# Optimization experiments

Measured on AMD Instinct MI355X. Metric: run time of the kernel, lower is better.

## Reference

```python
import jax, jax.numpy as jnp
import numpy as np

N = 50000      # nodes
E = 800000     # edges (avg degree 16)
C = 5000       # clusters (Kongming compression)
D = 128        # in_features
OUT = 40       # out_features (classes)
K = 2          # propagation hops


def setup_inputs() -> dict:
    key = jax.random.key(0)
    k1, k2, k3, k4, k5, k6 = jax.random.split(key, 6)
    x = jax.random.normal(k1, (N, D), dtype=jnp.float32)
    edge_index = jax.random.randint(k2, (2, E), 0, N, dtype=jnp.int32)
    cluster_index = jax.random.randint(k3, (N,), 0, C, dtype=jnp.int32)
    rep_idx = jax.random.randint(k4, (C,), 0, N, dtype=jnp.int32)
    W = jax.random.normal(k5, (OUT, D), dtype=jnp.float32) / np.sqrt(D)
    b = jax.random.normal(k6, (OUT,), dtype=jnp.float32) * 0.01
    return {"x": x, "edge_index": edge_index, "cluster_index": cluster_index,
            "rep_idx": rep_idx, "W": W, "b": b}


def _gcn_propagate(x, edge_index, k_hops):
    # PUPropagate: K hops of D^{-1/2}(A+I)D^{-1/2} x (gcn_norm with self-loops)
    n = x.shape[0]
    loops = jnp.arange(n, dtype=edge_index.dtype)
    src = jnp.concatenate([edge_index[0], loops])
    dst = jnp.concatenate([edge_index[1], loops])
    deg = jax.ops.segment_sum(jnp.ones_like(src, dtype=x.dtype), dst, num_segments=n)
    dinv = jnp.where(deg > 0, jax.lax.rsqrt(deg), 0.0)
    norm = (dinv[src] * dinv[dst])[:, None]            # [E+N, 1]
    h = x
    for _ in range(k_hops):                            # small fixed hop count
        h = jax.ops.segment_sum(h[src] * norm, dst, num_segments=n)
    return h


def reference(x, edge_index, cluster_index, rep_idx, W, b):
    h = _gcn_propagate(x, edge_index, K)               # [N, D]
    # Kongming_Cluster: gather one representative row per cluster
    hc = h[rep_idx]                                    # [C, D]
    yc = hc @ W.T + b                                  # [C, OUT] dense linear on compressed rows
    # Kongming_Reconstruct: scatter back to all nodes by cluster index
    y = yc[cluster_index]                              # [N, OUT]
    return jax.nn.log_softmax(y, axis=1)
```

## Files before the change

### kernel.cpp

```cpp
#include <hip/hip_runtime.h>
#include <math.h>

#define N_NODES 50000
#define N_EDGES 800000
#define N_CLUST 5000
#define DIM     128
#define NOUT    40
#define SLOTS   64
#define CSLOT   64

#define NBKT    391
#define BCAP    2560
#define GB_STR  16
#define BUCKB   250
#define EPB4    800

#define ZB     782
#define INVB   50
#define GRID_A (ZB + INVB + BUCKB)

typedef __attribute__((ext_vector_type(8))) short short8;
typedef __attribute__((ext_vector_type(4))) float fvec4;
typedef __attribute__((ext_vector_type(4))) int ivec4;

__device__ __forceinline__ short bf16r(float v) {
    unsigned u = __float_as_uint(v);
    u = (u + 0x7FFFu + ((u >> 16) & 1u)) >> 16;
    return (short)u;
}
__device__ __forceinline__ unsigned pack_bf16x2(float a, float b) {
    unsigned ua = __float_as_uint(a);
    unsigned ub = __float_as_uint(b);
    ua = (ua + 0x7FFFu + ((ua >> 16) & 1u)) >> 16;
    ub = (ub + 0x7FFFu + ((ub >> 16) & 1u)) >> 16;
    return ua | (ub << 16);
}
__device__ __forceinline__ float2 unpack_bf16x2(unsigned v) {
    float2 r;
    r.x = __uint_as_float(v << 16);
    r.y = __uint_as_float(v & 0xFFFF0000u);
    return r;
}
__device__ __forceinline__ float4 unpack_bf16x4(uint2 v) {
    float4 r;
    r.x = __uint_as_float(v.x << 16);
    r.y = __uint_as_float(v.x & 0xFFFF0000u);
    r.z = __uint_as_float(v.y << 16);
    r.w = __uint_as_float(v.y & 0xFFFF0000u);
    return r;
}
struct f8 { float4 a, b; };
__device__ __forceinline__ f8 unpack_bf16x8(uint4 q) {
    f8 r;
    r.a.x = __uint_as_float(q.x << 16);
    r.a.y = __uint_as_float(q.x & 0xFFFF0000u);
    r.a.z = __uint_as_float(q.y << 16);
    r.a.w = __uint_as_float(q.y & 0xFFFF0000u);
    r.b.x = __uint_as_float(q.z << 16);
    r.b.y = __uint_as_float(q.z & 0xFFFF0000u);
    r.b.z = __uint_as_float(q.w << 16);
    r.b.w = __uint_as_float(q.w & 0xFFFF0000u);
    return r;
}
__device__ __forceinline__ float4 sel4(bool c, float4 v) {
    float4 r;
    r.x = c ? v.x : 0.0f; r.y = c ? v.y : 0.0f;
    r.z = c ? v.z : 0.0f; r.w = c ? v.w : 0.0f;
    return r;
}

__global__ __launch_bounds__(256) void fused_A(const float* __restrict__ x,
                                               const int* __restrict__ esrc,
                                               const int* __restrict__ edst,
                                               const int* __restrict__ cidx,
                                               const float* __restrict__ W,
                                               int* __restrict__ ccnt,
                                               unsigned short* __restrict__ zs,
                                               unsigned short* __restrict__ cinv,
                                               int* __restrict__ gbcnt,
                                               unsigned* __restrict__ gbuck) {
    __shared__ int bcnt[NBKT];
    __shared__ int bbase[NBKT];
    int lane = threadIdx.x & 63;
    int wv = threadIdx.x >> 6;

    if (blockIdx.x < ZB) {
        int gw = blockIdx.x * 4 + wv;
        if (gw >= N_NODES / 16) return;
        int q = lane >> 4, r16 = lane & 15;

        short8 bfr[3][4];
        #pragma unroll
        for (int t = 0; t < 3; t++) {
            int o = t * 16 + r16;
            #pragma unroll
            for (int s = 0; s < 4; s++) {
                short8 f = {0, 0, 0, 0, 0, 0, 0, 0};
                if (o < NOUT) {
                    const float* wp = W + o * DIM + s * 32 + q * 8;
                    float4 w0 = *(const float4*)wp;
                    float4 w1 = *(const float4*)(wp + 4);
                    f[0] = bf16r(w0.x); f[1] = bf16r(w0.y);
                    f[2] = bf16r(w0.z); f[3] = bf16r(w0.w);
                    f[4] = bf16r(w1.x); f[5] = bf16r(w1.y);
                    f[6] = bf16r(w1.z); f[7] = bf16r(w1.w);
                }
                bfr[t][s] = f;
            }
        }

        int tile = gw;
        int node = tile * 16 + r16;
        short8 af[4];
        #pragma unroll
        for (int s = 0; s < 4; s++) {
            const fvec4* xp = (const fvec4*)(x + (size_t)node * DIM + s * 32 + q * 8);
            fvec4 a0 = *xp;
            fvec4 a1 = *(xp + 1);
            short8 f;
            f[0] = bf16r(a0.x); f[1] = bf16r(a0.y);
            f[2] = bf16r(a0.z); f[3] = bf16r(a0.w);
            f[4] = bf16r(a1.x); f[5] = bf16r(a1.y);
            f[6] = bf16r(a1.z); f[7] = bf16r(a1.w);
            af[s] = f;
        }

        fvec4 acc0 = {0, 0, 0, 0}, acc1 = {0, 0, 0, 0}, acc2 = {0, 0, 0, 0};
        #pragma unroll
        for (int s = 0; s < 4; s++) {
            acc0 = __builtin_amdgcn_mfma_f32_16x16x32_bf16(af[s], bfr[0][s], acc0, 0, 0, 0);
            acc1 = __builtin_amdgcn_mfma_f32_16x16x32_bf16(af[s], bfr[1][s], acc1, 0, 0, 0);
            acc2 = __builtin_amdgcn_mfma_f32_16x16x32_bf16(af[s], bfr[2][s], acc2, 0, 0, 0);
        }

        #pragma unroll
        for (int r = 0; r < 4; r++) {
            int nd = tile * 16 + q * 4 + r;
            unsigned short* zrow = zs + (size_t)nd * NOUT;
            __builtin_nontemporal_store((unsigned short)bf16r(acc0[r]), &zrow[r16]);
            __builtin_nontemporal_store((unsigned short)bf16r(acc1[r]), &zrow[16 + r16]);
            if (r16 < 8)
                __builtin_nontemporal_store((unsigned short)bf16r(acc2[r]), &zrow[32 + r16]);
        }
    } else if (blockIdx.x < ZB + INVB) {
        int t0 = (blockIdx.x - ZB) * 256 + threadIdx.x;
        for (int i = t0; i < N_NODES; i += INVB * 256) {
            int c = cidx[i];
            int pos = atomicAdd(&ccnt[c], 1);
            if (pos < CSLOT) cinv[c * CSLOT + pos] = (unsigned short)i;
        }
    } else {
        int fb = blockIdx.x - ZB - INVB;
        const ivec4* src4 = (const ivec4*)esrc;
        const ivec4* dst4 = (const ivec4*)edst;
        int q0 = fb * EPB4;

        for (int i = threadIdx.x; i < NBKT; i += 256) bcnt[i] = 0;
        __syncthreads();

        for (int i = threadIdx.x; i < EPB4; i += 256) {
            ivec4 d4 = dst4[q0 + i];
            atomicAdd(&bcnt[d4.x >> 7], 1);
            atomicAdd(&bcnt[d4.y >> 7], 1);
            atomicAdd(&bcnt[d4.z >> 7], 1);
            atomicAdd(&bcnt[d4.w >> 7], 1);
        }
        __syncthreads();

        for (int bk = threadIdx.x; bk < NBKT; bk += 256) {
            int c = bcnt[bk];
            bbase[bk] = c ? atomicAdd(&gbcnt[bk * GB_STR], c) : 0;
        }
        __syncthreads();
        for (int i = threadIdx.x; i < NBKT; i += 256) bcnt[i] = 0;
        __syncthreads();

        for (int i = threadIdx.x; i < EPB4; i += 256) {
            ivec4 d4 = dst4[q0 + i];
            ivec4 s4 = src4[q0 + i];
            {
                int bk = d4.x >> 7; int idx = atomicAdd(&bcnt[bk], 1);
                unsigned p = (unsigned)(bbase[bk] + idx);
                if (p < BCAP) gbuck[(size_t)bk * BCAP + p] = ((unsigned)d4.x << 16) | (unsigned)s4.x;
            }
            {
                int bk = d4.y >> 7; int idx = atomicAdd(&bcnt[bk], 1);
                unsigned p = (unsigned)(bbase[bk] + idx);
                if (p < BCAP) gbuck[(size_t)bk * BCAP + p] = ((unsigned)d4.y << 16) | (unsigned)s4.y;
            }
            {
                int bk = d4.z >> 7; int idx = atomicAdd(&bcnt[bk], 1);
                unsigned p = (unsigned)(bbase[bk] + idx);
                if (p < BCAP) gbuck[(size_t)bk * BCAP + p] = ((unsigned)d4.z << 16) | (unsigned)s4.z;
            }
            {
                int bk = d4.w >> 7; int idx = atomicAdd(&bcnt[bk], 1);
                unsigned p = (unsigned)(bbase[bk] + idx);
                if (p < BCAP) gbuck[(size_t)bk * BCAP + p] = ((unsigned)d4.w << 16) | (unsigned)s4.w;
            }
        }
    }
}

__global__ __launch_bounds__(256) void build_scale(const unsigned* __restrict__ gbuck,
                                                   const int* __restrict__ gbcnt,
                                                   const uint2* __restrict__ zs2,
                                                   int* __restrict__ cnt,
                                                   unsigned short* __restrict__ slot,
                                                   uint2* __restrict__ zd2) {
    __shared__ int c128[128];
    int b = blockIdx.x;
    if (threadIdx.x < 128) c128[threadIdx.x] = 0;
    __syncthreads();
    int m = gbcnt[b * GB_STR];
    if (m > BCAP) m = BCAP;
    const unsigned* bk = gbuck + (size_t)b * BCAP;
    for (int i = threadIdx.x; i < m; i += 256) {
        unsigned e = bk[i];
        int d7 = (int)(e >> 16) & 127;
        int pos = atomicAdd(&c128[d7], 1);
        if (pos < SLOTS)
            slot[((size_t)((b << 7) + d7)) * SLOTS + pos] = (unsigned short)(e & 0xFFFFu);
    }
    __syncthreads();
    int n0 = b << 7;
    if (threadIdx.x < 128) {
        int n = n0 + threadIdx.x;
        if (n < N_NODES) cnt[n] = c128[threadIdx.x];
    }
    for (int i = threadIdx.x; i < 128 * 10; i += 256) {
        int r = i / 10;
        int n = n0 + r;
        if (n < N_NODES) {
            int k = i - r * 10;
            float dn = rsqrtf((float)(c128[r] + 1));
            float4 f = unpack_bf16x4(zs2[(size_t)n * 10 + k]);
            uint2 p;
            p.x = pack_bf16x2(dn * f.x, dn * f.y);
            p.y = pack_bf16x2(dn * f.z, dn * f.w);
            zd2[(size_t)n * 10 + k] = p;
        }
    }
}

__global__ __launch_bounds__(256) void hop_all(const uint4* __restrict__ zd4,
                                               uint4* __restrict__ v14,
                                               const uint4* __restrict__ slot4,
                                               const int* __restrict__ cnt) {
    int lane = threadIdx.x & 63;
    int wv = threadIdx.x >> 6;
    int g = lane / 5;
    int k = lane - g * 5;
    int n = blockIdx.x * 48 + wv * 12 + g;
    if (g >= 12 || n >= N_NODES) return;
    int c = cnt[n];
    int m = (c < SLOTS) ? c : SLOTS;
    float s = 1.0f / (float)(c + 1);
    f8 self = unpack_bf16x8(zd4[(size_t)n * 5 + k]);
    float4 aA = self.a, aB = self.b;
    float4 bA = {0, 0, 0, 0}, bB = {0, 0, 0, 0};
    const uint4* srow = slot4 + (size_t)n * 8;
    int j = 0;
    for (; j + 8 <= m; j += 8) {
        uint4 s8 = srow[j >> 3];
        f8 f0 = unpack_bf16x8(zd4[(size_t)(s8.x & 0xFFFFu) * 5 + k]);
        f8 f1 = unpack_bf16x8(zd4[(size_t)(s8.x >> 16) * 5 + k]);
        f8 f2 = unpack_bf16x8(zd4[(size_t)(s8.y & 0xFFFFu) * 5 + k]);
        f8 f3 = unpack_bf16x8(zd4[(size_t)(s8.y >> 16) * 5 + k]);
        f8 f4 = unpack_bf16x8(zd4[(size_t)(s8.z & 0xFFFFu) * 5 + k]);
        f8 f5 = unpack_bf16x8(zd4[(size_t)(s8.z >> 16) * 5 + k]);
        f8 f6 = unpack_bf16x8(zd4[(size_t)(s8.w & 0xFFFFu) * 5 + k]);
        f8 f7 = unpack_bf16x8(zd4[(size_t)(s8.w >> 16) * 5 + k]);
        aA = aA + ((f0.a + f1.a) + (f4.a + f5.a));
        aB = aB + ((f0.b + f1.b) + (f4.b + f5.b));
        bA = bA + ((f2.a + f3.a) + (f6.a + f7.a));
        bB = bB + ((f2.b + f3.b) + (f6.b + f7.b));
    }
    if (j < m) {
        int rem = m - j;
        uint4 s8 = srow[j >> 3];
        unsigned i0 = s8.x & 0xFFFFu;
        unsigned i1 = (rem > 1) ? (s8.x >> 16) : 0u;
        unsigned i2 = (rem > 2) ? (s8.y & 0xFFFFu) : 0u;
        unsigned i3 = (rem > 3) ? (s8.y >> 16) : 0u;
        unsigned i4 = (rem > 4) ? (s8.z & 0xFFFFu) : 0u;
        unsigned i5 = (rem > 5) ? (s8.z >> 16) : 0u;
        unsigned i6 = (rem > 6) ? (s8.w & 0xFFFFu) : 0u;
        f8 f0 = unpack_bf16x8(zd4[(size_t)i0 * 5 + k]);
        f8 f1 = unpack_bf16x8(zd4[(size_t)i1 * 5 + k]);
        f8 f2 = unpack_bf16x8(zd4[(size_t)i2 * 5 + k]);
        f8 f3 = unpack_bf16x8(zd4[(size_t)i3 * 5 + k]);
        f8 f4 = unpack_bf16x8(zd4[(size_t)i4 * 5 + k]);
        f8 f5 = unpack_bf16x8(zd4[(size_t)i5 * 5 + k]);
        f8 f6 = unpack_bf16x8(zd4[(size_t)i6 * 5 + k]);
        aA = aA + f0.a;
        aB = aB + f0.b;
        bA = bA + sel4(rem > 1, f1.a) + sel4(rem > 3, f3.a) + sel4(rem > 5, f5.a);
        bB = bB + sel4(rem > 1, f1.b) + sel4(rem > 3, f3.b) + sel4(rem > 5, f5.b);
        aA = aA + sel4(rem > 2, f2.a) + sel4(rem > 4, f4.a) + sel4(rem > 6, f6.a);
        aB = aB + sel4(rem > 2, f2.b) + sel4(rem > 4, f4.b) + sel4(rem > 6, f6.b);
    }
    float4 rA = aA + bA;
    float4 rB = aB + bB;
    uint4 o;
    o.x = pack_bf16x2(s * rA.x, s * rA.y);
    o.y = pack_bf16x2(s * rA.z, s * rA.w);
    o.z = pack_bf16x2(s * rB.x, s * rB.y);
    o.w = pack_bf16x2(s * rB.z, s * rB.w);
    v14[(size_t)n * 5 + k] = o;
}

__global__ __launch_bounds__(256) void rep_scatter(const unsigned* __restrict__ v1,
                                                   const unsigned short* __restrict__ slot,
                                                   const int* __restrict__ cnt,
                                                   const int* __restrict__ ccnt,
                                                   const unsigned short* __restrict__ cinv,
                                                   const int* __restrict__ rep_idx,
                                                   const float2* __restrict__ b2,
                                                   float2* __restrict__ out2) {
    int lane = threadIdx.x & 63;
    int wv = threadIdx.x >> 6;
    int c = blockIdx.x * 4 + wv;
    if (c >= N_CLUST) return;
    int n = rep_idx[c];
    int cn = cnt[n];
    int m = (cn < SLOTS) ? cn : SLOTS;
    float dn = rsqrtf((float)(cn + 1));
    int g = lane / 20;
    int k = lane - g * 20;
    float2 acc; acc.x = 0.0f; acc.y = 0.0f;
    if (g == 0) acc = unpack_bf16x2(v1[n * 20 + k]);
    if (g < 3) {
        int base = n * SLOTS;
        for (int j = g; j < m; j += 3) {
            float2 f = unpack_bf16x2(v1[(int)slot[base + j] * 20 + k]);
            acc.x += f.x; acc.y += f.y;
        }
    }
    float t1x = __shfl(acc.x, lane + 20), t1y = __shfl(acc.y, lane + 20);
    float t2x = __shfl(acc.x, lane + 40), t2y = __shfl(acc.y, lane + 40);
    bool act = (lane < 20);
    float2 h; h.x = 0.0f; h.y = 0.0f;
    if (act) {
        float2 bb = b2[k];
        h.x = dn * (acc.x + t1x + t2x) + bb.x;
        h.y = dn * (acc.y + t1y + t2y) + bb.y;
    }
    float mx = act ? fmaxf(h.x, h.y) : -INFINITY;
    #pragma unroll
    for (int off = 32; off; off >>= 1) mx = fmaxf(mx, __shfl_xor(mx, off));
    float e = act ? (expf(h.x - mx) + expf(h.y - mx)) : 0.0f;
    #pragma unroll
    for (int off = 32; off; off >>= 1) e += __shfl_xor(e, off);
    float lg = mx + logf(e);
    float2 o; o.x = h.x - lg; o.y = h.y - lg;
    int mc = ccnt[c];
    if (mc > CSLOT) mc = CSLOT;
    const unsigned short* mem = cinv + c * CSLOT;
    for (int idx = 0; idx < mc; idx++) {
        int node = (int)mem[idx];
        if (act) out2[(size_t)node * 20 + k] = o;
    }
}

extern "C" void kernel_launch(void* const* d_in, const int* in_sizes, int n_in,
                              void* d_out, int out_size, void* d_ws, size_t ws_size,
                              hipStream_t stream) {
    const float* x    = (const float*)d_in[0];
    const int*   esrc = (const int*)d_in[1];
    const int*   edst = ((const int*)d_in[1]) + N_EDGES;
    const int*   cidx = (const int*)d_in[2];
    const int*   ridx = (const int*)d_in[3];
    const float* W    = (const float*)d_in[4];
    const float* b    = (const float*)d_in[5];
    float* out = (float*)d_out;

    char* ws = (char*)d_ws;
    size_t off = 0;
    auto alloc = [&](size_t bytes) { char* p = ws + off; off += (bytes + 255) & ~size_t(255); return p; };
    int*            cnt   = (int*)alloc((N_NODES + N_CLUST + NBKT * GB_STR) * 4);
    int*            ccnt  = cnt + N_NODES;
    int*            gbcnt = ccnt + N_CLUST;
    unsigned short* slot  = (unsigned short*)alloc((size_t)N_NODES * SLOTS * 2);
    unsigned short* zs    = (unsigned short*)alloc((size_t)N_NODES * NOUT * 2);
    unsigned short* zd    = (unsigned short*)alloc((size_t)N_NODES * NOUT * 2);
    unsigned*       v1    = (unsigned*)alloc((size_t)N_NODES * (NOUT / 2) * 4);
    unsigned short* cinv  = (unsigned short*)alloc((size_t)N_CLUST * CSLOT * 2);
    unsigned*       gbuck = (unsigned*)alloc((size_t)NBKT * BCAP * 4);
    (void)ws_size; (void)in_sizes; (void)n_in; (void)out_size;

    hipMemsetAsync(ccnt, 0, (N_CLUST + NBKT * GB_STR) * 4, stream);

    fused_A<<<GRID_A, 256, 0, stream>>>(x, esrc, edst, cidx, W,
                                        ccnt, zs, cinv, gbcnt, gbuck);
    build_scale<<<NBKT, 256, 0, stream>>>(gbuck, gbcnt, (const uint2*)zs,
                                          cnt, slot, (uint2*)zd);
    hop_all<<<(N_NODES + 47) / 48, 256, 0, stream>>>((const uint4*)zd, (uint4*)v1,
                                                     (const uint4*)slot, cnt);
    rep_scatter<<<(N_CLUST + 3) / 4, 256, 0, stream>>>((const unsigned*)v1, slot, cnt,
                                                       ccnt, cinv, ridx,
                                                       (const float2*)b, (float2*)out);
}
```

Measured before the change: 142.0 us.

## Fuse four kernels into one persistent kernel with software grid barriers

Merges the four launches (projection/bucketing, slot build and scaling, hop aggregation, representative scatter) into a single persistent kernel of 768 blocks. The phases are separated by atomic-counter grid barriers, and grid-stride loops replace the per-launch grids. The aim is to remove the launch gaps and tail effects between the small dependent kernels. In exchange, the barriers rely on all 768 blocks being co-resident (launch_bounds 256,4) and add spin-wait cost, with a deadlock risk if residency is not met.

```diff
diff --git a/kernel.cpp b/kernel.cpp
--- a/kernel.cpp
+++ b/kernel.cpp
@@ -15,9 +15,9 @@
 #define BUCKB   250
 #define EPB4    800
 
-#define ZB     782
-#define INVB   50
-#define GRID_A (ZB + INVB + BUCKB)
+#define GRID_F  768
+#define NWAVE   (GRID_F * 4)
+#define NTILE   (N_NODES / 16)
 
 typedef __attribute__((ext_vector_type(8))) short short8;
 typedef __attribute__((ext_vector_type(4))) float fvec4;
@@ -69,26 +69,45 @@
     return r;
 }
 
-__global__ __launch_bounds__(256) void fused_A(const float* __restrict__ x,
+__device__ __forceinline__ void gbar(int* bar, int target) {
+    __syncthreads();
+    if (threadIdx.x == 0) {
+        __threadfence();
+        atomicAdd(bar, 1);
+        while (atomicAdd(bar, 0) < target) {}
+        __threadfence();
+    }
+    __syncthreads();
+}
+
+__global__ __launch_bounds__(256, 4) void mega(const float* __restrict__ x,
                                                const int* __restrict__ esrc,
                                                const int* __restrict__ edst,
                                                const int* __restrict__ cidx,
+                                               const int* __restrict__ rep_idx,
                                                const float* __restrict__ W,
+                                               const float2* __restrict__ b2,
+                                               int* __restrict__ cnt,
                                                int* __restrict__ ccnt,
+                                               int* __restrict__ gbcnt,
+                                               unsigned short* __restrict__ slot,
                                                unsigned short* __restrict__ zs,
+                                               unsigned short* __restrict__ zd,
+                                               unsigned* __restrict__ v1,
                                                unsigned short* __restrict__ cinv,
-                                               int* __restrict__ gbcnt,
-                                               unsigned* __restrict__ gbuck) {
-    __shared__ int bcnt[NBKT];
-    __shared__ int bbase[NBKT];
-    int lane = threadIdx.x & 63;
-    int wv = threadIdx.x >> 6;
-
-    if (blockIdx.x < ZB) {
-        int gw = blockIdx.x * 4 + wv;
-        if (gw >= N_NODES / 16) return;
+                                               unsigned* __restrict__ gbuck,
+                                               int* __restrict__ bar,
+                                               float2* __restrict__ out2) {
+    __shared__ int shA[NBKT];
+    __shared__ int shB[NBKT];
+    int tid = threadIdx.x;
+    int lane = tid & 63;
+    int wv = tid >> 6;
+    int b = blockIdx.x;
+    int wave_id = b * 4 + wv;
+
+    {
         int q = lane >> 4, r16 = lane & 15;
-
         short8 bfr[3][4];
         #pragma unroll
         for (int t = 0; t < 3; t++) {
@@ -108,258 +127,242 @@
                 bfr[t][s] = f;
             }
         }
-
-        int tile = gw;
-        int node = tile * 16 + r16;
-        short8 af[4];
+        for (int tile = wave_id; tile < NTILE; tile += NWAVE) {
+            int node = tile * 16 + r16;
+            short8 af[4];
+            #pragma unroll
+            for (int s = 0; s < 4; s++) {
+                const fvec4* xp = (const fvec4*)(x + (size_t)node * DIM + s * 32 + q * 8);
+                fvec4 a0 = *xp;
+                fvec4 a1 = *(xp + 1);
+                short8 f;
+                f[0] = bf16r(a0.x); f[1] = bf16r(a0.y);
+                f[2] = bf16r(a0.z); f[3] = bf16r(a0.w);
+                f[4] = bf16r(a1.x); f[5] = bf16r(a1.y);
+                f[6] = bf16r(a1.z); f[7] = bf16r(a1.w);
+                af[s] = f;
+            }
+            fvec4 acc0 = {0, 0, 0, 0}, acc1 = {0, 0, 0, 0}, acc2 = {0, 0, 0, 0};
+            #pragma unroll
+            for (int s = 0; s < 4; s++) {
+                acc0 = __builtin_amdgcn_mfma_f32_16x16x32_bf16(af[s], bfr[0][s], acc0, 0, 0, 0);
+                acc1 = __builtin_amdgcn_mfma_f32_16x16x32_bf16(af[s], bfr[1][s], acc1, 0, 0, 0);
+                acc2 = __builtin_amdgcn_mfma_f32_16x16x32_bf16(af[s], bfr[2][s], acc2, 0, 0, 0);
+            }
+            #pragma unroll
+            for (int r = 0; r < 4; r++) {
+                int nd = tile * 16 + q * 4 + r;
+                unsigned short* zrow = zs + (size_t)nd * NOUT;
+                __builtin_nontemporal_store((unsigned short)bf16r(acc0[r]), &zrow[r16]);
+                __builtin_nontemporal_store((unsigned short)bf16r(acc1[r]), &zrow[16 + r16]);
+                if (r16 < 8)
+                    __builtin_nontemporal_store((unsigned short)bf16r(acc2[r]), &zrow[32 + r16]);
+            }
+        }
+
+        if (b < BUCKB) {
+            const ivec4* src4 = (const ivec4*)esrc;
+            const ivec4* dst4 = (const ivec4*)edst;
+            int q0 = b * EPB4;
+
+            for (int i = tid; i < NBKT; i += 256) shA[i] = 0;
+            __syncthreads();
+            for (int i = tid; i < EPB4; i += 256) {
+                ivec4 d4 = dst4[q0 + i];
+                atomicAdd(&shA[d4.x >> 7], 1);
+                atomicAdd(&shA[d4.y >> 7], 1);
+                atomicAdd(&shA[d4.z >> 7], 1);
+                atomicAdd(&shA[d4.w >> 7], 1);
+            }
+            __syncthreads();
+            for (int bk = tid; bk < NBKT; bk += 256) {
+                int c = shA[bk];
+                shB[bk] = c ? atomicAdd(&gbcnt[bk * GB_STR], c) : 0;
+            }
+            __syncthreads();
+            for (int i = tid; i < NBKT; i += 256) shA[i] = 0;
+            __syncthreads();
+            for (int i = tid; i < EPB4; i += 256) {
+                ivec4 d4 = dst4[q0 + i];
+                ivec4 s4 = src4[q0 + i];
+                {
+                    int bk = d4.x >> 7; int idx = atomicAdd(&shA[bk], 1);
+                    unsigned p = (unsigned)(shB[bk] + idx);
+                    if (p < BCAP) gbuck[(size_t)bk * BCAP + p] = ((unsigned)d4.x << 16) | (unsigned)s4.x;
+                }
+                {
+                    int bk = d4.y >> 7; int idx = atomicAdd(&shA[bk], 1);
+                    unsigned p = (unsigned)(shB[bk] + idx);
+                    if (p < BCAP) gbuck[(size_t)bk * BCAP + p] = ((unsigned)d4.y << 16) | (unsigned)s4.y;
+                }
+                {
+                    int bk = d4.z >> 7; int idx = atomicAdd(&shA[bk], 1);
+                    unsigned p = (unsigned)(shB[bk] + idx);
+                    if (p < BCAP) gbuck[(size_t)bk * BCAP + p] = ((unsigned)d4.z << 16) | (unsigned)s4.z;
+                }
+                {
+                    int bk = d4.w >> 7; int idx = atomicAdd(&shA[bk], 1);
+                    unsigned p = (unsigned)(shB[bk] + idx);
+                    if (p < BCAP) gbuck[(size_t)bk * BCAP + p] = ((unsigned)d4.w << 16) | (unsigned)s4.w;
+                }
+            }
+        } else if (b >= 256 && b < 256 + 196) {
+            int i = (b - 256) * 256 + tid;
+            if (i < N_NODES) {
+                int c = cidx[i];
+                int pos = atomicAdd(&ccnt[c], 1);
+                if (pos < CSLOT) cinv[c * CSLOT + pos] = (unsigned short)i;
+            }
+        }
+    }
+    gbar(bar, GRID_F);
+
+    if (b < NBKT) {
+        const uint2* zs2 = (const uint2*)zs;
+        uint2* zd2 = (uint2*)zd;
+        if (tid < 128) shA[tid] = 0;
+        __syncthreads();
+        int m = gbcnt[b * GB_STR];
+        if (m > BCAP) m = BCAP;
+        const unsigned* bk = gbuck + (size_t)b * BCAP;
+        for (int i = tid; i < m; i += 256) {
+            unsigned e = bk[i];
+            int d7 = (int)(e >> 16) & 127;
+            int pos = atomicAdd(&shA[d7], 1);
+            if (pos < SLOTS)
+                slot[((size_t)((b << 7) + d7)) * SLOTS + pos] = (unsigned short)(e & 0xFFFFu);
+        }
+        __syncthreads();
+        int n0 = b << 7;
+        if (tid < 128) {
+            int n = n0 + tid;
+            if (n < N_NODES) cnt[n] = shA[tid];
+        }
+        for (int i = tid; i < 128 * 10; i += 256) {
+            int r = i / 10;
+            int n = n0 + r;
+            if (n < N_NODES) {
+                int k = i - r * 10;
+                float dn = rsqrtf((float)(shA[r] + 1));
+                float4 f = unpack_bf16x4(zs2[(size_t)n * 10 + k]);
+                uint2 p;
+                p.x = pack_bf16x2(dn * f.x, dn * f.y);
+                p.y = pack_bf16x2(dn * f.z, dn * f.w);
+                zd2[(size_t)n * 10 + k] = p;
+            }
+        }
+    }
+    gbar(bar, GRID_F * 2);
+
+    {
+        const uint4* zd4 = (const uint4*)zd;
+        uint4* v14 = (uint4*)v1;
+        const uint4* slot4 = (const uint4*)slot;
+        int g = lane / 5;
+        int k = lane - g * 5;
+        for (int n0 = wave_id * 12; n0 < N_NODES; n0 += NWAVE * 12) {
+            int n = n0 + g;
+            if (g < 12 && n < N_NODES) {
+                int c = cnt[n];
+                int m = (c < SLOTS) ? c : SLOTS;
+                float s = 1.0f / (float)(c + 1);
+                f8 self = unpack_bf16x8(zd4[(size_t)n * 5 + k]);
+                float4 aA = self.a, aB = self.b;
+                float4 bA = {0, 0, 0, 0}, bB = {0, 0, 0, 0};
+                const uint4* srow = slot4 + (size_t)n * 8;
+                int j = 0;
+                for (; j + 8 <= m; j += 8) {
+                    uint4 s8 = srow[j >> 3];
+                    f8 f0 = unpack_bf16x8(zd4[(size_t)(s8.x & 0xFFFFu) * 5 + k]);
+                    f8 f1 = unpack_bf16x8(zd4[(size_t)(s8.x >> 16) * 5 + k]);
+                    f8 f2 = unpack_bf16x8(zd4[(size_t)(s8.y & 0xFFFFu) * 5 + k]);
+                    f8 f3 = unpack_bf16x8(zd4[(size_t)(s8.y >> 16) * 5 + k]);
+                    f8 f4 = unpack_bf16x8(zd4[(size_t)(s8.z & 0xFFFFu) * 5 + k]);
+                    f8 f5 = unpack_bf16x8(zd4[(size_t)(s8.z >> 16) * 5 + k]);
+                    f8 f6 = unpack_bf16x8(zd4[(size_t)(s8.w & 0xFFFFu) * 5 + k]);
+                    f8 f7 = unpack_bf16x8(zd4[(size_t)(s8.w >> 16) * 5 + k]);
+                    aA = aA + ((f0.a + f1.a) + (f4.a + f5.a));
+                    aB = aB + ((f0.b + f1.b) + (f4.b + f5.b));
+                    bA = bA + ((f2.a + f3.a) + (f6.a + f7.a));
+                    bB = bB + ((f2.b + f3.b) + (f6.b + f7.b));
+                }
+                if (j < m) {
+                    int rem = m - j;
+                    uint4 s8 = srow[j >> 3];
+                    unsigned i0 = s8.x & 0xFFFFu;
+                    unsigned i1 = (rem > 1) ? (s8.x >> 16) : 0u;
+                    unsigned i2 = (rem > 2) ? (s8.y & 0xFFFFu) : 0u;
+                    unsigned i3 = (rem > 3) ? (s8.y >> 16) : 0u;
+                    unsigned i4 = (rem > 4) ? (s8.z & 0xFFFFu) : 0u;
+                    unsigned i5 = (rem > 5) ? (s8.z >> 16) : 0u;
+                    unsigned i6 = (rem > 6) ? (s8.w & 0xFFFFu) : 0u;
+                    f8 f0 = unpack_bf16x8(zd4[(size_t)i0 * 5 + k]);
+                    f8 f1 = unpack_bf16x8(zd4[(size_t)i1 * 5 + k]);
+                    f8 f2 = unpack_bf16x8(zd4[(size_t)i2 * 5 + k]);
+                    f8 f3 = unpack_bf16x8(zd4[(size_t)i3 * 5 + k]);
+                    f8 f4 = unpack_bf16x8(zd4[(size_t)i4 * 5 + k]);
+                    f8 f5 = unpack_bf16x8(zd4[(size_t)i5 * 5 + k]);
+                    f8 f6 = unpack_bf16x8(zd4[(size_t)i6 * 5 + k]);
+                    aA = aA + f0.a;
+                    aB = aB + f0.b;
+                    bA = bA + sel4(rem > 1, f1.a) + sel4(rem > 3, f3.a) + sel4(rem > 5, f5.a);
+                    bB = bB + sel4(rem > 1, f1.b) + sel4(rem > 3, f3.b) + sel4(rem > 5, f5.b);
+                    aA = aA + sel4(rem > 2, f2.a) + sel4(rem > 4, f4.a) + sel4(rem > 6, f6.a);
+                    aB = aB + sel4(rem > 2, f2.b) + sel4(rem > 4, f4.b) + sel4(rem > 6, f6.b);
+                }
+                float4 rA = aA + bA;
+                float4 rB = aB + bB;
+                uint4 o;
+                o.x = pack_bf16x2(s * rA.x, s * rA.y);
+                o.y = pack_bf16x2(s * rA.z, s * rA.w);
+                o.z = pack_bf16x2(s * rB.x, s * rB.y);
+                o.w = pack_bf16x2(s * rB.z, s * rB.w);
+                v14[(size_t)n * 5 + k] = o;
+            }
+        }
+    }
+    gbar(bar, GRID_F * 3);
+
+    for (int c = wave_id; c < N_CLUST; c += NWAVE) {
+        int n = rep_idx[c];
+        int cn = cnt[n];
+        int m = (cn < SLOTS) ? cn : SLOTS;
+        float dn = rsqrtf((float)(cn + 1));
+        int g = lane / 20;
+        int k = lane - g * 20;
+        float2 acc; acc.x = 0.0f; acc.y = 0.0f;
+        if (g == 0) acc = unpack_bf16x2(v1[n * 20 + k]);
+        if (g < 3) {
+            int base = n * SLOTS;
+            for (int j = g; j < m; j += 3) {
+                float2 f = unpack_bf16x2(v1[(int)slot[base + j] * 20 + k]);
+                acc.x += f.x; acc.y += f.y;
+            }
+        }
+        float t1x = __shfl(acc.x, lane + 20), t1y = __shfl(acc.y, lane + 20);
+        float t2x = __shfl(acc.x, lane + 40), t2y = __shfl(acc.y, lane + 40);
+        bool act = (lane < 20);
+        float2 h; h.x = 0.0f; h.y = 0.0f;
+        if (act) {
+            float2 bb = b2[k];
+            h.x = dn * (acc.x + t1x + t2x) + bb.x;
+            h.y = dn * (acc.y + t1y + t2y) + bb.y;
+        }
+        float mx = act ? fmaxf(h.x, h.y) : -INFINITY;
         #pragma unroll
-        for (int s = 0; s < 4; s++) {
-            const fvec4* xp = (const fvec4*)(x + (size_t)node * DIM + s * 32 + q * 8);
-            fvec4 a0 = *xp;
-            fvec4 a1 = *(xp + 1);
-            short8 f;
-            f[0] = bf16r(a0.x); f[1] = bf16r(a0.y);
-            f[2] = bf16r(a0.z); f[3] = bf16r(a0.w);
-            f[4] = bf16r(a1.x); f[5] = bf16r(a1.y);
-            f[6] = bf16r(a1.z); f[7] = bf16r(a1.w);
-            af[s] = f;
-        }
-
-        fvec4 acc0 = {0, 0, 0, 0}, acc1 = {0, 0, 0, 0}, acc2 = {0, 0, 0, 0};
+        for (int off = 32; off; off >>= 1) mx = fmaxf(mx, __shfl_xor(mx, off));
+        float e = act ? (expf(h.x - mx) + expf(h.y - mx)) : 0.0f;
         #pragma unroll
-        for (int s = 0; s < 4; s++) {
-            acc0 = __builtin_amdgcn_mfma_f32_16x16x32_bf16(af[s], bfr[0][s], acc0, 0, 0, 0);
-            acc1 = __builtin_amdgcn_mfma_f32_16x16x32_bf16(af[s], bfr[1][s], acc1, 0, 0, 0);
-            acc2 = __builtin_amdgcn_mfma_f32_16x16x32_bf16(af[s], bfr[2][s], acc2, 0, 0, 0);
-        }
-
-        #pragma unroll
-        for (int r = 0; r < 4; r++) {
-            int nd = tile * 16 + q * 4 + r;
-            unsigned short* zrow = zs + (size_t)nd * NOUT;
-            __builtin_nontemporal_store((unsigned short)bf16r(acc0[r]), &zrow[r16]);
-            __builtin_nontemporal_store((unsigned short)bf16r(acc1[r]), &zrow[16 + r16]);
-            if (r16 < 8)
-                __builtin_nontemporal_store((unsigned short)bf16r(acc2[r]), &zrow[32 + r16]);
-        }
-    } else if (blockIdx.x < ZB + INVB) {
-        int t0 = (blockIdx.x - ZB) * 256 + threadIdx.x;
-        for (int i = t0; i < N_NODES; i += INVB * 256) {
-            int c = cidx[i];
-            int pos = atomicAdd(&ccnt[c], 1);
-            if (pos < CSLOT) cinv[c * CSLOT + pos] = (unsigned short)i;
-        }
-    } else {
-        int fb = blockIdx.x - ZB - INVB;
-        const ivec4* src4 = (const ivec4*)esrc;
-        const ivec4* dst4 = (const ivec4*)edst;
-        int q0 = fb * EPB4;
-
-        for (int i = threadIdx.x; i < NBKT; i += 256) bcnt[i] = 0;
-        __syncthreads();
-
-        for (int i = threadIdx.x; i < EPB4; i += 256) {
-            ivec4 d4 = dst4[q0 + i];
-            atomicAdd(&bcnt[d4.x >> 7], 1);
-            atomicAdd(&bcnt[d4.y >> 7], 1);
-            atomicAdd(&bcnt[d4.z >> 7], 1);
-            atomicAdd(&bcnt[d4.w >> 7], 1);
-        }
-        __syncthreads();
-
-        for (int bk = threadIdx.x; bk < NBKT; bk += 256) {
-            int c = bcnt[bk];
-            bbase[bk] = c ? atomicAdd(&gbcnt[bk * GB_STR], c) : 0;
-        }
-        __syncthreads();
-        for (int i = threadIdx.x; i < NBKT; i += 256) bcnt[i] = 0;
-        __syncthreads();
-
-        for (int i = threadIdx.x; i < EPB4; i += 256) {
-            ivec4 d4 = dst4[q0 + i];
-            ivec4 s4 = src4[q0 + i];
-            {
-                int bk = d4.x >> 7; int idx = atomicAdd(&bcnt[bk], 1);
-                unsigned p = (unsigned)(bbase[bk] + idx);
-                if (p < BCAP) gbuck[(size_t)bk * BCAP + p] = ((unsigned)d4.x << 16) | (unsigned)s4.x;
-            }
-            {
-                int bk = d4.y >> 7; int idx = atomicAdd(&bcnt[bk], 1);
-                unsigned p = (unsigned)(bbase[bk] + idx);
-                if (p < BCAP) gbuck[(size_t)bk * BCAP + p] = ((unsigned)d4.y << 16) | (unsigned)s4.y;
-            }
-            {
-                int bk = d4.z >> 7; int idx = atomicAdd(&bcnt[bk], 1);
-                unsigned p = (unsigned)(bbase[bk] + idx);
-                if (p < BCAP) gbuck[(size_t)bk * BCAP + p] = ((unsigned)d4.z << 16) | (unsigned)s4.z;
-            }
-            {
-                int bk = d4.w >> 7; int idx = atomicAdd(&bcnt[bk], 1);
-                unsigned p = (unsigned)(bbase[bk] + idx);
-                if (p < BCAP) gbuck[(size_t)bk * BCAP + p] = ((unsigned)d4.w << 16) | (unsigned)s4.w;
-            }
-        }
-    }
-}
-
-__global__ __launch_bounds__(256) void build_scale(const unsigned* __restrict__ gbuck,
-                                                   const int* __restrict__ gbcnt,
-                                                   const uint2* __restrict__ zs2,
-                                                   int* __restrict__ cnt,
-                                                   unsigned short* __restrict__ slot,
-                                                   uint2* __restrict__ zd2) {
-    __shared__ int c128[128];
-    int b = blockIdx.x;
-    if (threadIdx.x < 128) c128[threadIdx.x] = 0;
-    __syncthreads();
-    int m = gbcnt[b * GB_STR];
-    if (m > BCAP) m = BCAP;
-    const unsigned* bk = gbuck + (size_t)b * BCAP;
-    for (int i = threadIdx.x; i < m; i += 256) {
-        unsigned e = bk[i];
-        int d7 = (int)(e >> 16) & 127;
-        int pos = atomicAdd(&c128[d7], 1);
-        if (pos < SLOTS)
-            slot[((size_t)((b << 7) + d7)) * SLOTS + pos] = (unsigned short)(e & 0xFFFFu);
-    }
-    __syncthreads();
-    int n0 = b << 7;
-    if (threadIdx.x < 128) {
-        int n = n0 + threadIdx.x;
-        if (n < N_NODES) cnt[n] = c128[threadIdx.x];
-    }
-    for (int i = threadIdx.x; i < 128 * 10; i += 256) {
-        int r = i / 10;
-        int n = n0 + r;
-        if (n < N_NODES) {
-            int k = i - r * 10;
-            float dn = rsqrtf((float)(c128[r] + 1));
-            float4 f = unpack_bf16x4(zs2[(size_t)n * 10 + k]);
-            uint2 p;
-            p.x = pack_bf16x2(dn * f.x, dn * f.y);
-            p.y = pack_bf16x2(dn * f.z, dn * f.w);
-            zd2[(size_t)n * 10 + k] = p;
-        }
-    }
-}
-
-__global__ __launch_bounds__(256) void hop_all(const uint4* __restrict__ zd4,
-                                               uint4* __restrict__ v14,
-                                               const uint4* __restrict__ slot4,
-                                               const int* __restrict__ cnt) {
-    int lane = threadIdx.x & 63;
-    int wv = threadIdx.x >> 6;
-    int g = lane / 5;
-    int k = lane - g * 5;
-    int n = blockIdx.x * 48 + wv * 12 + g;
-    if (g >= 12 || n >= N_NODES) return;
-    int c = cnt[n];
-    int m = (c < SLOTS) ? c : SLOTS;
-    float s = 1.0f / (float)(c + 1);
-    f8 self = unpack_bf16x8(zd4[(size_t)n * 5 + k]);
-    float4 aA = self.a, aB = self.b;
-    float4 bA = {0, 0, 0, 0}, bB = {0, 0, 0, 0};
-    const uint4* srow = slot4 + (size_t)n * 8;
-    int j = 0;
-    for (; j + 8 <= m; j += 8) {
-        uint4 s8 = srow[j >> 3];
-        f8 f0 = unpack_bf16x8(zd4[(size_t)(s8.x & 0xFFFFu) * 5 + k]);
-        f8 f1 = unpack_bf16x8(zd4[(size_t)(s8.x >> 16) * 5 + k]);
-        f8 f2 = unpack_bf16x8(zd4[(size_t)(s8.y & 0xFFFFu) * 5 + k]);
-        f8 f3 = unpack_bf16x8(zd4[(size_t)(s8.y >> 16) * 5 + k]);
-        f8 f4 = unpack_bf16x8(zd4[(size_t)(s8.z & 0xFFFFu) * 5 + k]);
-        f8 f5 = unpack_bf16x8(zd4[(size_t)(s8.z >> 16) * 5 + k]);
-        f8 f6 = unpack_bf16x8(zd4[(size_t)(s8.w & 0xFFFFu) * 5 + k]);
-        f8 f7 = unpack_bf16x8(zd4[(size_t)(s8.w >> 16) * 5 + k]);
-        aA = aA + ((f0.a + f1.a) + (f4.a + f5.a));
-        aB = aB + ((f0.b + f1.b) + (f4.b + f5.b));
-        bA = bA + ((f2.a + f3.a) + (f6.a + f7.a));
-        bB = bB + ((f2.b + f3.b) + (f6.b + f7.b));
-    }
-    if (j < m) {
-        int rem = m - j;
-        uint4 s8 = srow[j >> 3];
-        unsigned i0 = s8.x & 0xFFFFu;
-        unsigned i1 = (rem > 1) ? (s8.x >> 16) : 0u;
-        unsigned i2 = (rem > 2) ? (s8.y & 0xFFFFu) : 0u;
-        unsigned i3 = (rem > 3) ? (s8.y >> 16) : 0u;
-        unsigned i4 = (rem > 4) ? (s8.z & 0xFFFFu) : 0u;
-        unsigned i5 = (rem > 5) ? (s8.z >> 16) : 0u;
-        unsigned i6 = (rem > 6) ? (s8.w & 0xFFFFu) : 0u;
-        f8 f0 = unpack_bf16x8(zd4[(size_t)i0 * 5 + k]);
-        f8 f1 = unpack_bf16x8(zd4[(size_t)i1 * 5 + k]);
-        f8 f2 = unpack_bf16x8(zd4[(size_t)i2 * 5 + k]);
-        f8 f3 = unpack_bf16x8(zd4[(size_t)i3 * 5 + k]);
-        f8 f4 = unpack_bf16x8(zd4[(size_t)i4 * 5 + k]);
-        f8 f5 = unpack_bf16x8(zd4[(size_t)i5 * 5 + k]);
-        f8 f6 = unpack_bf16x8(zd4[(size_t)i6 * 5 + k]);
-        aA = aA + f0.a;
-        aB = aB + f0.b;
-        bA = bA + sel4(rem > 1, f1.a) + sel4(rem > 3, f3.a) + sel4(rem > 5, f5.a);
-        bB = bB + sel4(rem > 1, f1.b) + sel4(rem > 3, f3.b) + sel4(rem > 5, f5.b);
-        aA = aA + sel4(rem > 2, f2.a) + sel4(rem > 4, f4.a) + sel4(rem > 6, f6.a);
-        aB = aB + sel4(rem > 2, f2.b) + sel4(rem > 4, f4.b) + sel4(rem > 6, f6.b);
-    }
-    float4 rA = aA + bA;
-    float4 rB = aB + bB;
-    uint4 o;
-    o.x = pack_bf16x2(s * rA.x, s * rA.y);
-    o.y = pack_bf16x2(s * rA.z, s * rA.w);
-    o.z = pack_bf16x2(s * rB.x, s * rB.y);
-    o.w = pack_bf16x2(s * rB.z, s * rB.w);
-    v14[(size_t)n * 5 + k] = o;
-}
-
-__global__ __launch_bounds__(256) void rep_scatter(const unsigned* __restrict__ v1,
-                                                   const unsigned short* __restrict__ slot,
-                                                   const int* __restrict__ cnt,
-                                                   const int* __restrict__ ccnt,
-                                                   const unsigned short* __restrict__ cinv,
-                                                   const int* __restrict__ rep_idx,
-                                                   const float2* __restrict__ b2,
-                                                   float2* __restrict__ out2) {
-    int lane = threadIdx.x & 63;
-    int wv = threadIdx.x >> 6;
-    int c = blockIdx.x * 4 + wv;
-    if (c >= N_CLUST) return;
-    int n = rep_idx[c];
-    int cn = cnt[n];
-    int m = (cn < SLOTS) ? cn : SLOTS;
-    float dn = rsqrtf((float)(cn + 1));
-    int g = lane / 20;
-    int k = lane - g * 20;
-    float2 acc; acc.x = 0.0f; acc.y = 0.0f;
-    if (g == 0) acc = unpack_bf16x2(v1[n * 20 + k]);
-    if (g < 3) {
-        int base = n * SLOTS;
-        for (int j = g; j < m; j += 3) {
-            float2 f = unpack_bf16x2(v1[(int)slot[base + j] * 20 + k]);
-            acc.x += f.x; acc.y += f.y;
-        }
-    }
-    float t1x = __shfl(acc.x, lane + 20), t1y = __shfl(acc.y, lane + 20);
-    float t2x = __shfl(acc.x, lane + 40), t2y = __shfl(acc.y, lane + 40);
-    bool act = (lane < 20);
-    float2 h; h.x = 0.0f; h.y = 0.0f;
-    if (act) {
-        float2 bb = b2[k];
-        h.x = dn * (acc.x + t1x + t2x) + bb.x;
-        h.y = dn * (acc.y + t1y + t2y) + bb.y;
-    }
-    float mx = act ? fmaxf(h.x, h.y) : -INFINITY;
-    #pragma unroll
-    for (int off = 32; off; off >>= 1) mx = fmaxf(mx, __shfl_xor(mx, off));
-    float e = act ? (expf(h.x - mx) + expf(h.y - mx)) : 0.0f;
-    #pragma unroll
-    for (int off = 32; off; off >>= 1) e += __shfl_xor(e, off);
-    float lg = mx + logf(e);
-    float2 o; o.x = h.x - lg; o.y = h.y - lg;
-    int mc = ccnt[c];
-    if (mc > CSLOT) mc = CSLOT;
-    const unsigned short* mem = cinv + c * CSLOT;
-    for (int idx = 0; idx < mc; idx++) {
-        int node = (int)mem[idx];
-        if (act) out2[(size_t)node * 20 + k] = o;
+        for (int off = 32; off; off >>= 1) e += __shfl_xor(e, off);
+        float lg = mx + logf(e);
+        float2 o; o.x = h.x - lg; o.y = h.y - lg;
+        int mc = ccnt[c];
+        if (mc > CSLOT) mc = CSLOT;
+        const unsigned short* mem = cinv + c * CSLOT;
+        for (int idx = 0; idx < mc; idx++) {
+            int node = (int)mem[idx];
+            if (act) out2[(size_t)node * 20 + k] = o;
+        }
     }
 }
 
@@ -378,9 +381,10 @@
     char* ws = (char*)d_ws;
     size_t off = 0;
     auto alloc = [&](size_t bytes) { char* p = ws + off; off += (bytes + 255) & ~size_t(255); return p; };
-    int*            cnt   = (int*)alloc((N_NODES + N_CLUST + NBKT * GB_STR) * 4);
+    int*            cnt   = (int*)alloc((N_NODES + N_CLUST + NBKT * GB_STR + 64) * 4);
     int*            ccnt  = cnt + N_NODES;
     int*            gbcnt = ccnt + N_CLUST;
+    int*            bar   = gbcnt + NBKT * GB_STR;
     unsigned short* slot  = (unsigned short*)alloc((size_t)N_NODES * SLOTS * 2);
     unsigned short* zs    = (unsigned short*)alloc((size_t)N_NODES * NOUT * 2);
     unsigned short* zd    = (unsigned short*)alloc((size_t)N_NODES * NOUT * 2);
@@ -389,15 +393,10 @@
     unsigned*       gbuck = (unsigned*)alloc((size_t)NBKT * BCAP * 4);
     (void)ws_size; (void)in_sizes; (void)n_in; (void)out_size;
 
-    hipMemsetAsync(ccnt, 0, (N_CLUST + NBKT * GB_STR) * 4, stream);
-
-    fused_A<<<GRID_A, 256, 0, stream>>>(x, esrc, edst, cidx, W,
-                                        ccnt, zs, cinv, gbcnt, gbuck);
-    build_scale<<<NBKT, 256, 0, stream>>>(gbuck, gbcnt, (const uint2*)zs,
-                                          cnt, slot, (uint2*)zd);
-    hop_all<<<(N_NODES + 47) / 48, 256, 0, stream>>>((const uint4*)zd, (uint4*)v1,
-                                                     (const uint4*)slot, cnt);
-    rep_scatter<<<(N_CLUST + 3) / 4, 256, 0, stream>>>((const unsigned*)v1, slot, cnt,
-                                                       ccnt, cinv, ridx,
-                                                       (const float2*)b, (float2*)out);
-}
+    hipMemsetAsync(ccnt, 0, (N_CLUST + NBKT * GB_STR + 64) * 4, stream);
+
+    mega<<<GRID_F, 256, 0, stream>>>(x, esrc, edst, cidx, ridx, W,
+                                     (const float2*)b,
+                                     cnt, ccnt, gbcnt, slot, zs, zd, v1, cinv,
+                                     gbuck, bar, (float2*)out);
+}
```

After: 404.7 us. +185.0%, slower.

## Stage slot lists in LDS, add nontemporal hints, spread output writes across lanes

Applied to the files above, without the earlier changes.

build_scale now builds each bucket's 128x64 slot table in shared memory and writes it out to global with coalesced 16-byte nontemporal stores, replacing scattered 2-byte global stores. The edge bucketing loads and stores in fused_A use nontemporal builtins so the streaming data bypasses cache retention. The final scatter in rep_scatter broadcasts the result through shuffles so three lane groups write different cluster members in parallel, instead of only 20 active lanes per member. The cost is 16KB of extra LDS per block and full-row slot writes, which include unused entries that were previously never written.

```diff
diff --git a/kernel.cpp b/kernel.cpp
--- a/kernel.cpp
+++ b/kernel.cpp
@@ -22,6 +22,7 @@
 typedef __attribute__((ext_vector_type(8))) short short8;
 typedef __attribute__((ext_vector_type(4))) float fvec4;
 typedef __attribute__((ext_vector_type(4))) int ivec4;
+typedef __attribute__((ext_vector_type(4))) unsigned uvec4;
 
 __device__ __forceinline__ short bf16r(float v) {
     unsigned u = __float_as_uint(v);
@@ -176,27 +177,31 @@
         __syncthreads();
 
         for (int i = threadIdx.x; i < EPB4; i += 256) {
-            ivec4 d4 = dst4[q0 + i];
-            ivec4 s4 = src4[q0 + i];
+            ivec4 d4 = __builtin_nontemporal_load(&dst4[q0 + i]);
+            ivec4 s4 = __builtin_nontemporal_load(&src4[q0 + i]);
             {
                 int bk = d4.x >> 7; int idx = atomicAdd(&bcnt[bk], 1);
                 unsigned p = (unsigned)(bbase[bk] + idx);
-                if (p < BCAP) gbuck[(size_t)bk * BCAP + p] = ((unsigned)d4.x << 16) | (unsigned)s4.x;
+                if (p < BCAP) __builtin_nontemporal_store(((unsigned)d4.x << 16) | (unsigned)s4.x,
+                                                          &gbuck[(size_t)bk * BCAP + p]);
             }
             {
                 int bk = d4.y >> 7; int idx = atomicAdd(&bcnt[bk], 1);
                 unsigned p = (unsigned)(bbase[bk] + idx);
-                if (p < BCAP) gbuck[(size_t)bk * BCAP + p] = ((unsigned)d4.y << 16) | (unsigned)s4.y;
+                if (p < BCAP) __builtin_nontemporal_store(((unsigned)d4.y << 16) | (unsigned)s4.y,
+                                                          &gbuck[(size_t)bk * BCAP + p]);
             }
             {
                 int bk = d4.z >> 7; int idx = atomicAdd(&bcnt[bk], 1);
                 unsigned p = (unsigned)(bbase[bk] + idx);
-                if (p < BCAP) gbuck[(size_t)bk * BCAP + p] = ((unsigned)d4.z << 16) | (unsigned)s4.z;
+                if (p < BCAP) __builtin_nontemporal_store(((unsigned)d4.z << 16) | (unsigned)s4.z,
+                                                          &gbuck[(size_t)bk * BCAP + p]);
             }
             {
                 int bk = d4.w >> 7; int idx = atomicAdd(&bcnt[bk], 1);
                 unsigned p = (unsigned)(bbase[bk] + idx);
-                if (p < BCAP) gbuck[(size_t)bk * BCAP + p] = ((unsigned)d4.w << 16) | (unsigned)s4.w;
+                if (p < BCAP) __builtin_nontemporal_store(((unsigned)d4.w << 16) | (unsigned)s4.w,
+                                                          &gbuck[(size_t)bk * BCAP + p]);
             }
         }
     }
@@ -209,26 +214,36 @@
                                                    unsigned short* __restrict__ slot,
                                                    uint2* __restrict__ zd2) {
     __shared__ int c128[128];
+    __shared__ unsigned short sl[128 * SLOTS];
+    int tid = threadIdx.x;
     int b = blockIdx.x;
-    if (threadIdx.x < 128) c128[threadIdx.x] = 0;
+    if (tid < 128) c128[tid] = 0;
     __syncthreads();
     int m = gbcnt[b * GB_STR];
     if (m > BCAP) m = BCAP;
     const unsigned* bk = gbuck + (size_t)b * BCAP;
-    for (int i = threadIdx.x; i < m; i += 256) {
-        unsigned e = bk[i];
+    for (int i = tid; i < m; i += 256) {
+        unsigned e = __builtin_nontemporal_load(&bk[i]);
         int d7 = (int)(e >> 16) & 127;
         int pos = atomicAdd(&c128[d7], 1);
-        if (pos < SLOTS)
-            slot[((size_t)((b << 7) + d7)) * SLOTS + pos] = (unsigned short)(e & 0xFFFFu);
+        if (pos < SLOTS) sl[(d7 << 6) + pos] = (unsigned short)(e & 0xFFFFu);
     }
     __syncthreads();
+    {
+        int rows = N_NODES - (b << 7);
+        if (rows > 128) rows = 128;
+        int n4 = rows * (SLOTS / 8);
+        const uvec4* s4 = (const uvec4*)sl;
+        uvec4* g4 = (uvec4*)(slot + ((size_t)(b << 7)) * SLOTS);
+        for (int i = tid; i < n4; i += 256)
+            __builtin_nontemporal_store(s4[i], &g4[i]);
+    }
     int n0 = b << 7;
-    if (threadIdx.x < 128) {
-        int n = n0 + threadIdx.x;
-        if (n < N_NODES) cnt[n] = c128[threadIdx.x];
-    }
-    for (int i = threadIdx.x; i < 128 * 10; i += 256) {
+    if (tid < 128) {
+        int n = n0 + tid;
+        if (n < N_NODES) cnt[n] = c128[tid];
+    }
+    for (int i = tid; i < 128 * 10; i += 256) {
         int r = i / 10;
         int n = n0 + r;
         if (n < N_NODES) {
@@ -354,12 +369,17 @@
     for (int off = 32; off; off >>= 1) e += __shfl_xor(e, off);
     float lg = mx + logf(e);
     float2 o; o.x = h.x - lg; o.y = h.y - lg;
+    float ox = __shfl(o.x, k);
+    float oy = __shfl(o.y, k);
     int mc = ccnt[c];
     if (mc > CSLOT) mc = CSLOT;
     const unsigned short* mem = cinv + c * CSLOT;
-    for (int idx = 0; idx < mc; idx++) {
-        int node = (int)mem[idx];
-        if (act) out2[(size_t)node * 20 + k] = o;
+    if (g < 3) {
+        float2 ob; ob.x = ox; ob.y = oy;
+        for (int idx = g; idx < mc; idx += 3) {
+            int node = (int)mem[idx];
+            out2[(size_t)node * 20 + k] = ob;
+        }
     }
 }
 
@@ -389,7 +409,7 @@
     unsigned*       gbuck = (unsigned*)alloc((size_t)NBKT * BCAP * 4);
     (void)ws_size; (void)in_sizes; (void)n_in; (void)out_size;
 
-    hipMemsetAsync(ccnt, 0, (N_CLUST + NBKT * GB_STR) * 4, stream);
+    (void)hipMemsetAsync(ccnt, 0, (N_CLUST + NBKT * GB_STR) * 4, stream);
 
     fused_A<<<GRID_A, 256, 0, stream>>>(x, esrc, edst, cidx, W,
                                         ccnt, zs, cinv, gbcnt, gbuck);
```

Result: slower. 154.4 us (+8.7%).
